# Performance work log

Hardware: AMD Instinct MI355X
Metric: run time of the kernel (lower is better)

Reference implementation:

```python
import jax, jax.numpy as jnp
import numpy as np

# Mamba hyperparameters (match init_kwargs)
DIM = 384
D_STATE = 16
D_CONV = 4
EXPAND = 2
D_INNER = EXPAND * DIM            # 768
DT_RANK = (DIM + 15) // 16        # ceil(dim/16) = 24


def setup_inputs() -> dict:
    key = jax.random.key(0)
    ks = jax.random.split(key, 9)
    B = 4
    img_dims = (16, 16, 16)
    s = 0.02
    x = jax.random.normal(ks[0], (B, DIM) + img_dims, dtype=jnp.float32)
    # LayerNorm params
    gamma = jnp.ones((DIM,), jnp.float32)
    beta = jnp.zeros((DIM,), jnp.float32)
    # Mamba params (torch Linear layout: (out, in))
    W_in = jax.random.normal(ks[1], (2 * D_INNER, DIM), jnp.float32) * s
    conv_w = jax.random.normal(ks[2], (D_INNER, 1, D_CONV), jnp.float32) * (D_CONV ** -0.5)
    conv_b = jnp.zeros((D_INNER,), jnp.float32)
    W_xproj = jax.random.normal(ks[3], (DT_RANK + 2 * D_STATE, D_INNER), jnp.float32) * s
    W_dt = jax.random.normal(ks[4], (D_INNER, DT_RANK), jnp.float32) * (DT_RANK ** -0.5)
    # bias init so softplus(b_dt) gives small positive dt (~0.02), like mamba_ssm
    b_dt = jnp.full((D_INNER,), -4.0, jnp.float32) + jax.random.normal(ks[5], (D_INNER,), jnp.float32) * 0.1
    # S4D-real init: A = -[1..d_state] per channel
    A_log = jnp.log(jnp.broadcast_to(jnp.arange(1, D_STATE + 1, dtype=jnp.float32), (D_INNER, D_STATE)))
    D = jnp.ones((D_INNER,), jnp.float32)
    W_out = jax.random.normal(ks[6], (DIM, D_INNER), jnp.float32) * s
    return {"x": x, "gamma": gamma, "beta": beta, "W_in": W_in, "conv_w": conv_w,
            "conv_b": conv_b, "W_xproj": W_xproj, "W_dt": W_dt, "b_dt": b_dt,
            "A_log": A_log, "D": D, "W_out": W_out}


def _mamba_layer(x, gamma, beta, W_in, conv_w, conv_b, W_xproj, W_dt, b_dt, A_log, D, W_out):
    B, C = x.shape[0], x.shape[1]
    img_dims = x.shape[2:]
    L = int(np.prod(img_dims))
    xf = x.reshape(B, C, L).transpose(0, 2, 1)          # (B, L, C)

    # LayerNorm over channel dim
    mu = xf.mean(-1, keepdims=True)
    xc = xf - mu
    var = (xc * xc).mean(-1, keepdims=True)
    xn = xc * jax.lax.rsqrt(var + 1e-5) * gamma + beta   # (B, L, C)

    # in_proj -> x, z branches
    xz = xn @ W_in.T                                     # (B, L, 2*D_INNER)
    xm, z = jnp.split(xz, 2, axis=-1)

    # causal depthwise conv1d + SiLU
    xcv = xm.transpose(0, 2, 1)                          # (B, D_INNER, L)
    conv = jax.lax.conv_general_dilated(
        xcv, conv_w, window_strides=(1,), padding=[(D_CONV - 1, 0)],
        feature_group_count=D_INNER) + conv_b[None, :, None]
    xm = jax.nn.silu(conv.transpose(0, 2, 1))            # (B, L, D_INNER)

    # input-dependent dt, B, C
    dbl = xm @ W_xproj.T                                 # (B, L, DT_RANK + 2*D_STATE)
    dt, Bm, Cm = jnp.split(dbl, [DT_RANK, DT_RANK + D_STATE], axis=-1)
    delta = jax.nn.softplus(dt @ W_dt.T + b_dt)          # (B, L, D_INNER)
    A = -jnp.exp(A_log)                                  # (D_INNER, D_STATE)

    # selective scan over time (time-major)
    def step(h, inp):
        d_t, x_t, B_t, C_t = inp                         # (B,Din),(B,Din),(B,Dst),(B,Dst)
        dA = jnp.exp(d_t[..., None] * A)                 # (B, D_INNER, D_STATE)
        h = h * dA + (d_t * x_t)[..., None] * B_t[:, None, :]
        y = jnp.einsum('bds,bs->bd', h, C_t)
        return h, y

    h0 = jnp.zeros((B, D_INNER, D_STATE), xm.dtype)
    inps = (delta.transpose(1, 0, 2), xm.transpose(1, 0, 2),
            Bm.transpose(1, 0, 2), Cm.transpose(1, 0, 2))
    _, ys = jax.lax.scan(step, h0, inps)                 # (L, B, D_INNER)

    y = ys.transpose(1, 0, 2) + xm * D                   # skip via D
    y = y * jax.nn.silu(z)                               # gate
    out = y @ W_out.T                                    # (B, L, C)
    return out.transpose(0, 2, 1).reshape(x.shape)


def reference(x, gamma, beta, W_in, conv_w, conv_b, W_xproj, W_dt, b_dt, A_log, D, W_out):
    return _mamba_layer(x, gamma, beta, W_in, conv_w, conv_b, W_xproj, W_dt, b_dt, A_log, D, W_out)
```

## Files before the change

### kernel.cpp

```cpp
#include <hip/hip_runtime.h>

typedef short v8s __attribute__((ext_vector_type(8)));
typedef float v4f __attribute__((ext_vector_type(4)));

#define LSEQ   4096
#define BATCH  4
#define NDIM   384
#define DIN    768
#define DST    16
#define DTR    24
#define NTOK   (BATCH * LSEQ)
#define NCHUNK 128
#define CLEN   32
#define CT     8

__device__ __forceinline__ float b2f(unsigned short u) {
  unsigned int v = ((unsigned int)u) << 16;
  float f; __builtin_memcpy(&f, &v, 4); return f;
}
__device__ __forceinline__ unsigned short f2b(float f) {
  unsigned int x; __builtin_memcpy(&x, &f, 4);
  unsigned int r = x + 0x7FFFu + ((x >> 16) & 1u);
  return (unsigned short)(r >> 16);
}
__device__ __forceinline__ void gl2lds16(const void* g, void* l) {
  __builtin_amdgcn_global_load_lds(
      (const __attribute__((address_space(1))) void*)g,
      (__attribute__((address_space(3))) void*)l, 16, 0, 0);
}

__global__ __launch_bounds__(256) void cast_w(
    const float* __restrict__ a, unsigned short* __restrict__ oa, int na,
    const float* __restrict__ b, unsigned short* __restrict__ ob, int nb,
    const float* __restrict__ c, unsigned short* __restrict__ oc, int nc,
    const float* __restrict__ wdt, unsigned short* __restrict__ odt)
{
  int i = blockIdx.x * 256 + threadIdx.x;
  if (i < na) oa[i] = f2b(a[i]);
  if (i < nb) ob[i] = f2b(b[i]);
  if (i < nc) oc[i] = f2b(c[i]);
  if (i < DIN * 32) {
    int n = i >> 5, r = i & 31;
    odt[i] = (r < DTR) ? f2b(wdt[n * DTR + r]) : (unsigned short)0;
  }
}

__global__ __launch_bounds__(256) void ln_stats(
    const float* __restrict__ x, float* __restrict__ mu, float* __restrict__ rs)
{
  __shared__ float red[512];
  int blk = blockIdx.x;
  int b = blk >> 7, lc = blk & 127;
  int l0 = lc * 32;
  int t = threadIdx.x;
  int lt = t & 31, part = t >> 5;
  float s = 0.f, ss = 0.f;
  for (int c = part; c < NDIM; c += 8) {
    float v = x[((size_t)b * NDIM + c) * LSEQ + l0 + lt];
    s += v; ss += v * v;
  }
  red[part * 32 + lt] = s;
  red[256 + part * 32 + lt] = ss;
  __syncthreads();
  if (t < 32) {
    float sum = 0.f, ssum = 0.f;
    #pragma unroll
    for (int k = 0; k < 8; k++) { sum += red[k * 32 + t]; ssum += red[256 + k * 32 + t]; }
    float m = sum / (float)NDIM;
    float var = ssum / (float)NDIM - m * m;
    mu[(size_t)b * LSEQ + l0 + t] = m;
    rs[(size_t)b * LSEQ + l0 + t] = rsqrtf(var + 1e-5f);
  }
}

__global__ __launch_bounds__(256) void ln_apply(
    const float* __restrict__ x, const float* __restrict__ mu,
    const float* __restrict__ rs, const float* __restrict__ gamma,
    const float* __restrict__ beta, unsigned short* __restrict__ xn)
{
  __shared__ unsigned short tile[64 * 66];
  int blk = blockIdx.x;
  int ltb = blk & 63, ct = (blk >> 6) % 6, b = blk / (6 * 64);
  int l0 = ltb * 64, c0 = ct * 64;
  int t = threadIdx.x;
  int col = (t & 15) * 4;
  float4 mu4 = *(const float4*)(mu + (size_t)b * LSEQ + l0 + col);
  float4 rs4 = *(const float4*)(rs + (size_t)b * LSEQ + l0 + col);
  #pragma unroll
  for (int p = 0; p < 4; p++) {
    int row = (t >> 4) + p * 16;
    float g = gamma[c0 + row], be = beta[c0 + row];
    float4 v = *(const float4*)(x + ((size_t)b * NDIM + c0 + row) * LSEQ + l0 + col);
    unsigned int u0 = (unsigned int)f2b((v.x - mu4.x) * rs4.x * g + be)
                    | ((unsigned int)f2b((v.y - mu4.y) * rs4.y * g + be) << 16);
    unsigned int u1 = (unsigned int)f2b((v.z - mu4.z) * rs4.z * g + be)
                    | ((unsigned int)f2b((v.w - mu4.w) * rs4.w * g + be) << 16);
    *(unsigned int*)&tile[row * 66 + col]     = u0;
    *(unsigned int*)&tile[row * 66 + col + 2] = u1;
  }
  __syncthreads();
  for (int idx = t; idx < 64 * 64; idx += 256) {
    int l = idx >> 6, c = idx & 63;
    xn[((size_t)b * LSEQ + l0 + l) * NDIM + c0 + c] = tile[c * 66 + l];
  }
}

template <typename OT>
__global__ __launch_bounds__(256) void gemm128(
    const unsigned short* __restrict__ A, const unsigned short* __restrict__ W,
    OT* __restrict__ C, int K, int ldc)
{
  __shared__ short As[128 * 32];
  __shared__ short Ws[128 * 32];
  int t = threadIdx.x;
  int wave = t >> 6, lane = t & 63;
  int m0 = blockIdx.x * 128, n0 = blockIdx.y * 128;
  int wm = wave >> 1, wn = wave & 1;
  int lrow = lane & 15, quad = lane >> 4;
  int l4 = lane >> 2, p = lane & 3;
  int row0 = wave * 32 + l4;
  int row1 = row0 + 16;
  int k8 = p ^ (row0 & 3);
  int ldsoff0 = wave * 1024 + lane * 8;
  int ldsoff1 = ldsoff0 + 512;
  int swz = (lrow & 3) * 8;
  v4f acc[4][4];
  #pragma unroll
  for (int i = 0; i < 4; i++)
    #pragma unroll
    for (int j = 0; j < 4; j++) acc[i][j] = (v4f){0.f, 0.f, 0.f, 0.f};
  for (int kk = 0; kk < K; kk += 32) {
    gl2lds16(A + (size_t)(m0 + row0) * K + kk + k8 * 8, &As[ldsoff0]);
    gl2lds16(A + (size_t)(m0 + row1) * K + kk + k8 * 8, &As[ldsoff1]);
    gl2lds16(W + (size_t)(n0 + row0) * K + kk + k8 * 8, &Ws[ldsoff0]);
    gl2lds16(W + (size_t)(n0 + row1) * K + kk + k8 * 8, &Ws[ldsoff1]);
    __syncthreads();
    v8s af[4], bf[4];
    #pragma unroll
    for (int i = 0; i < 4; i++) {
      int ra = wm * 64 + i * 16 + lrow;
      af[i] = *(const v8s*)&As[ra * 32 + ((quad * 8) ^ swz)];
    }
    #pragma unroll
    for (int j = 0; j < 4; j++) {
      int rb = wn * 64 + j * 16 + lrow;
      bf[j] = *(const v8s*)&Ws[rb * 32 + ((quad * 8) ^ swz)];
    }
    #pragma unroll
    for (int i = 0; i < 4; i++)
      #pragma unroll
      for (int j = 0; j < 4; j++)
        acc[i][j] = __builtin_amdgcn_mfma_f32_16x16x32_bf16(af[i], bf[j], acc[i][j], 0, 0, 0);
    __syncthreads();
  }
  #pragma unroll
  for (int i = 0; i < 4; i++) {
    #pragma unroll
    for (int j = 0; j < 4; j++) {
      #pragma unroll
      for (int r = 0; r < 4; r++) {
        int m = m0 + wm * 64 + i * 16 + quad * 4 + r;
        int n = n0 + wn * 64 + j * 16 + lrow;
        if constexpr (sizeof(OT) == 4) C[(size_t)m * ldc + n] = acc[i][j][r];
        else                           C[(size_t)m * ldc + n] = (OT)f2b(acc[i][j][r]);
      }
    }
  }
}

__global__ __launch_bounds__(256) void gemm_out(
    const unsigned short* __restrict__ A, const unsigned short* __restrict__ W,
    float* __restrict__ out, int K)
{
  __shared__ short As[128 * 32];
  __shared__ short Ws[128 * 32];
  int t = threadIdx.x;
  int wave = t >> 6, lane = t & 63;
  int m0 = blockIdx.x * 128, n0 = blockIdx.y * 128;
  int wm = wave >> 1, wn = wave & 1;
  int lrow = lane & 15, quad = lane >> 4;
  int l4 = lane >> 2, p = lane & 3;
  int row0 = wave * 32 + l4;
  int row1 = row0 + 16;
  int k8 = p ^ (row0 & 3);
  int ldsoff0 = wave * 1024 + lane * 8;
  int ldsoff1 = ldsoff0 + 512;
  int swz = (lrow & 3) * 8;
  v4f acc[4][4];
  #pragma unroll
  for (int i = 0; i < 4; i++)
    #pragma unroll
    for (int j = 0; j < 4; j++) acc[i][j] = (v4f){0.f, 0.f, 0.f, 0.f};
  for (int kk = 0; kk < K; kk += 32) {
    gl2lds16(A + (size_t)(m0 + row0) * K + kk + k8 * 8, &As[ldsoff0]);
    gl2lds16(A + (size_t)(m0 + row1) * K + kk + k8 * 8, &As[ldsoff1]);
    gl2lds16(W + (size_t)(n0 + row0) * K + kk + k8 * 8, &Ws[ldsoff0]);
    gl2lds16(W + (size_t)(n0 + row1) * K + kk + k8 * 8, &Ws[ldsoff1]);
    __syncthreads();
    v8s af[4], bf[4];
    #pragma unroll
    for (int i = 0; i < 4; i++) {
      int ra = wm * 64 + i * 16 + lrow;
      af[i] = *(const v8s*)&As[ra * 32 + ((quad * 8) ^ swz)];
    }
    #pragma unroll
    for (int j = 0; j < 4; j++) {
      int rb = wn * 64 + j * 16 + lrow;
      bf[j] = *(const v8s*)&Ws[rb * 32 + ((quad * 8) ^ swz)];
    }
    #pragma unroll
    for (int i = 0; i < 4; i++)
      #pragma unroll
      for (int j = 0; j < 4; j++)
        acc[i][j] = __builtin_amdgcn_mfma_f32_16x16x32_bf16(af[i], bf[j], acc[i][j], 0, 0, 0);
    __syncthreads();
  }
  #pragma unroll
  for (int i = 0; i < 4; i++) {
    #pragma unroll
    for (int j = 0; j < 4; j++) {
      #pragma unroll
      for (int r = 0; r < 4; r++) {
        int m = m0 + wm * 64 + i * 16 + quad * 4 + r;
        int n = n0 + wn * 64 + j * 16 + lrow;
        int b = n >> 12, l = n & (LSEQ - 1);
        out[((size_t)b * NDIM + m) * LSEQ + l] = acc[i][j][r];
      }
    }
  }
}

#define LDK 40
__global__ __launch_bounds__(256) void gemm_bt64(
    const unsigned short* __restrict__ A, const unsigned short* __restrict__ W,
    unsigned short* __restrict__ C, int Nw, int K, int ldc)
{
  __shared__ short As[64 * LDK];
  __shared__ short Ws[64 * LDK];
  int m0 = blockIdx.x * 64, n0 = blockIdx.y * 64;
  int t = threadIdx.x;
  int wave = t >> 6, lane = t & 63;
  int lrow = lane & 15, quad = lane >> 4;
  int ldrow = t >> 2, ldcg = t & 3;
  v4f acc[4];
  #pragma unroll
  for (int j = 0; j < 4; j++) acc[j] = (v4f){0.f, 0.f, 0.f, 0.f};
  for (int kk = 0; kk < K; kk += 32) {
    v8s av = *(const v8s*)(A + (size_t)(m0 + ldrow) * K + kk + ldcg * 8);
    *(v8s*)&As[ldrow * LDK + ldcg * 8] = av;
    int wrow = n0 + ldrow;
    v8s wv = {0, 0, 0, 0, 0, 0, 0, 0};
    if (wrow < Nw) wv = *(const v8s*)(W + (size_t)wrow * K + kk + ldcg * 8);
    *(v8s*)&Ws[ldrow * LDK + ldcg * 8] = wv;
    __syncthreads();
    v8s afrag = *(const v8s*)&As[(wave * 16 + lrow) * LDK + quad * 8];
    #pragma unroll
    for (int j = 0; j < 4; j++) {
      v8s bfrag = *(const v8s*)&Ws[(j * 16 + lrow) * LDK + quad * 8];
      acc[j] = __builtin_amdgcn_mfma_f32_16x16x32_bf16(afrag, bfrag, acc[j], 0, 0, 0);
    }
    __syncthreads();
  }
  #pragma unroll
  for (int j = 0; j < 4; j++) {
    #pragma unroll
    for (int r = 0; r < 4; r++) {
      int m = m0 + wave * 16 + quad * 4 + r;
      int n = n0 + j * 16 + lrow;
      if (n < ldc) C[(size_t)m * ldc + n] = f2b(acc[j][r]);
    }
  }
}

__global__ __launch_bounds__(256) void dt_gemm(
    const unsigned short* __restrict__ A, const unsigned short* __restrict__ W,
    const float* __restrict__ b_dt, unsigned short* __restrict__ delta)
{
  __shared__ short As[128 * 32];
  __shared__ short Ws[128 * 32];
  int t = threadIdx.x;
  int wave = t >> 6, lane = t & 63;
  int m0 = blockIdx.x * 128, n0 = blockIdx.y * 128;
  int wm = wave >> 1, wn = wave & 1;
  int lrow = lane & 15, quad = lane >> 4;
  int l4 = lane >> 2, p = lane & 3;
  int row0 = wave * 32 + l4;
  int row1 = row0 + 16;
  int k8 = p ^ (row0 & 3);
  int ldsoff0 = wave * 1024 + lane * 8;
  int ldsoff1 = ldsoff0 + 512;
  int swz = (lrow & 3) * 8;
  gl2lds16(A + (size_t)(m0 + row0) * 64 + k8 * 8, &As[ldsoff0]);
  gl2lds16(A + (size_t)(m0 + row1) * 64 + k8 * 8, &As[ldsoff1]);
  gl2lds16(W + (size_t)(n0 + row0) * 32 + k8 * 8, &Ws[ldsoff0]);
  gl2lds16(W + (size_t)(n0 + row1) * 32 + k8 * 8, &Ws[ldsoff1]);
  __syncthreads();
  v4f acc[4][4];
  #pragma unroll
  for (int i = 0; i < 4; i++)
    #pragma unroll
    for (int j = 0; j < 4; j++) acc[i][j] = (v4f){0.f, 0.f, 0.f, 0.f};
  v8s af[4], bf[4];
  #pragma unroll
  for (int i = 0; i < 4; i++) {
    int ra = wm * 64 + i * 16 + lrow;
    af[i] = *(const v8s*)&As[ra * 32 + ((quad * 8) ^ swz)];
  }
  #pragma unroll
  for (int j = 0; j < 4; j++) {
    int rb = wn * 64 + j * 16 + lrow;
    bf[j] = *(const v8s*)&Ws[rb * 32 + ((quad * 8) ^ swz)];
  }
  #pragma unroll
  for (int i = 0; i < 4; i++)
    #pragma unroll
    for (int j = 0; j < 4; j++)
      acc[i][j] = __builtin_amdgcn_mfma_f32_16x16x32_bf16(af[i], bf[j], acc[i][j], 0, 0, 0);
  #pragma unroll
  for (int j = 0; j < 4; j++) {
    int n = n0 + wn * 64 + j * 16 + lrow;
    float bb = b_dt[n];
    #pragma unroll
    for (int i = 0; i < 4; i++) {
      #pragma unroll
      for (int r = 0; r < 4; r++) {
        int m = m0 + wm * 64 + i * 16 + quad * 4 + r;
        float a = acc[i][j][r] + bb;
        float sp = (a > 20.f) ? a : __logf(1.f + __expf(a));
        delta[(size_t)m * DIN + n] = f2b(sp);
      }
    }
  }
}

__global__ __launch_bounds__(256) void conv_silu_w(
    const unsigned short* __restrict__ xz, const float* __restrict__ conv_w,
    const float* __restrict__ conv_b, unsigned short* __restrict__ xc)
{
  int idx = blockIdx.x * 256 + threadIdx.x;
  int dg = idx % (DIN / 8);
  int bl0 = idx / (DIN / 8);
  int d = dg * 8;
  int t0 = bl0 * CT;
  int l0 = t0 & (LSEQ - 1);
  float w[4][8], bb[8];
  #pragma unroll
  for (int e = 0; e < 8; e++) {
    float4 we = *(const float4*)(conv_w + (size_t)(d + e) * 4);
    w[0][e] = we.x; w[1][e] = we.y; w[2][e] = we.z; w[3][e] = we.w;
  }
  {
    float4 b0 = *(const float4*)(conv_b + d);
    float4 b1 = *(const float4*)(conv_b + d + 4);
    bb[0] = b0.x; bb[1] = b0.y; bb[2] = b0.z; bb[3] = b0.w;
    bb[4] = b1.x; bb[5] = b1.y; bb[6] = b1.z; bb[7] = b1.w;
  }
  float xw[3][8];
  #pragma unroll
  for (int j = 0; j < 3; j++) {
    if (l0 - 3 + j >= 0) {
      v8s v = *(const v8s*)(xz + (size_t)(t0 - 3 + j) * (2 * DIN) + d);
      #pragma unroll
      for (int e = 0; e < 8; e++) xw[j][e] = b2f((unsigned short)v[e]);
    } else {
      #pragma unroll
      for (int e = 0; e < 8; e++) xw[j][e] = 0.f;
    }
  }
  for (int tt = 0; tt < CT; tt++) {
    v8s v = *(const v8s*)(xz + (size_t)(t0 + tt) * (2 * DIN) + d);
    float cur[8];
    #pragma unroll
    for (int e = 0; e < 8; e++) cur[e] = b2f((unsigned short)v[e]);
    v8s o;
    #pragma unroll
    for (int e = 0; e < 8; e++) {
      float acc = bb[e];
      acc = __builtin_fmaf(w[0][e], xw[0][e], acc);
      acc = __builtin_fmaf(w[1][e], xw[1][e], acc);
      acc = __builtin_fmaf(w[2][e], xw[2][e], acc);
      acc = __builtin_fmaf(w[3][e], cur[e], acc);
      float sig = 1.f / (1.f + __expf(-acc));
      o[e] = (short)f2b(acc * sig);
    }
    *(v8s*)(xc + (size_t)(t0 + tt) * DIN + d) = o;
    #pragma unroll
    for (int e = 0; e < 8; e++) {
      xw[0][e] = xw[1][e]; xw[1][e] = xw[2][e]; xw[2][e] = cur[e];
    }
  }
}

__global__ __launch_bounds__(256) void scan_a(
    const unsigned short* __restrict__ delta, const unsigned short* __restrict__ xc,
    const unsigned short* __restrict__ dbl, const float* __restrict__ A_log,
    float* __restrict__ P, float* __restrict__ H)
{
  __shared__ float BCf[CLEN * 32];
  int blk = blockIdx.x;
  int q = blk % 3, c = (blk / 3) % NCHUNK, b = blk / (3 * NCHUNK);
  int t = threadIdx.x;
  int d = q * 256 + t;
  if (t < CLEN * 4) {
    int tt = t >> 2, g = t & 3;
    v8s raw = *(const v8s*)(dbl + (size_t)(b * LSEQ + c * CLEN + tt) * 64 + DTR + g * 8);
    float* dst = &BCf[tt * 32 + g * 8];
    #pragma unroll
    for (int e = 0; e < 8; e++) dst[e] = b2f((unsigned short)raw[e]);
  }
  __syncthreads();
  float A_d[DST];
  bool fast = true;
  #pragma unroll
  for (int s = 0; s < DST; s++) {
    A_d[s] = -__expf(A_log[d * DST + s]);
    fast = fast && (__builtin_fabsf(A_d[s] + (float)(s + 1)) < 1e-3f * (s + 1));
  }
  float h[DST];
  #pragma unroll
  for (int s = 0; s < DST; s++) h[s] = 0.f;
  float S = 0.f;
  size_t base = ((size_t)b * LSEQ + c * CLEN) * DIN + d;
  if (fast) {
    for (int tt = 0; tt < CLEN; tt++) {
      float du = b2f(delta[base + (size_t)tt * DIN]);
      float xv = b2f(xc[base + (size_t)tt * DIN]);
      float dx = du * xv;
      S += du;
      float r = __expf(-du);
      float Bv[16];
      #pragma unroll
      for (int g = 0; g < 4; g++)
        *(float4*)&Bv[g * 4] = *(const float4*)&BCf[tt * 32 + g * 4];
      float a = r;
      #pragma unroll
      for (int s = 0; s < DST; s++) {
        h[s] = __builtin_fmaf(h[s], a, dx * Bv[s]);
        a *= r;
      }
    }
  } else {
    for (int tt = 0; tt < CLEN; tt++) {
      float du = b2f(delta[base + (size_t)tt * DIN]);
      float xv = b2f(xc[base + (size_t)tt * DIN]);
      float dx = du * xv;
      S += du;
      #pragma unroll
      for (int s = 0; s < DST; s++) {
        float a = __expf(du * A_d[s]);
        h[s] = h[s] * a + dx * BCf[tt * 32 + s];
      }
    }
  }
  size_t obase = (((size_t)b * NCHUNK + c) * DST) * DIN + d;
  if (fast) {
    float rS = __expf(-S), a = rS;
    #pragma unroll
    for (int s = 0; s < DST; s++) { P[obase + (size_t)s * DIN] = a; a *= rS; }
  } else {
    #pragma unroll
    for (int s = 0; s < DST; s++) P[obase + (size_t)s * DIN] = __expf(A_d[s] * S);
  }
  #pragma unroll
  for (int s = 0; s < DST; s++) H[obase + (size_t)s * DIN] = h[s];
}

__global__ __launch_bounds__(256) void scan_b(
    const float* __restrict__ P, const float* __restrict__ H, float* __restrict__ Hstart)
{
  int i = blockIdx.x * 256 + threadIdx.x;
  if (i >= BATCH * DST * DIN) return;
  int d = i % DIN;
  int s = (i / DIN) % DST;
  int b = i / (DST * DIN);
  float h = 0.f;
  for (int c = 0; c < NCHUNK; c++) {
    size_t idx = (((size_t)b * NCHUNK + c) * DST + s) * DIN + d;
    float p = P[idx];
    float hh = H[idx];
    Hstart[idx] = h;
    h = h * p + hh;
  }
}

__global__ __launch_bounds__(256) void scan_c(
    const unsigned short* __restrict__ delta, const unsigned short* __restrict__ xc,
    const unsigned short* __restrict__ dbl, const float* __restrict__ A_log,
    const float* __restrict__ Hstart, const unsigned short* __restrict__ xz,
    const float* __restrict__ Dp, unsigned short* __restrict__ ygate)
{
  __shared__ float BCf[CLEN * 32];
  int blk = blockIdx.x;
  int q = blk % 3, c = (blk / 3) % NCHUNK, b = blk / (3 * NCHUNK);
  int t = threadIdx.x;
  int d = q * 256 + t;
  if (t < CLEN * 4) {
    int tt = t >> 2, g = t & 3;
    v8s raw = *(const v8s*)(dbl + (size_t)(b * LSEQ + c * CLEN + tt) * 64 + DTR + g * 8);
    float* dst = &BCf[tt * 32 + g * 8];
    #pragma unroll
    for (int e = 0; e < 8; e++) dst[e] = b2f((unsigned short)raw[e]);
  }
  __syncthreads();
  float A_d[DST];
  bool fast = true;
  #pragma unroll
  for (int s = 0; s < DST; s++) {
    A_d[s] = -__expf(A_log[d * DST + s]);
    fast = fast && (__builtin_fabsf(A_d[s] + (float)(s + 1)) < 1e-3f * (s + 1));
  }
  size_t obase = (((size_t)b * NCHUNK + c) * DST) * DIN + d;
  float h[DST];
  #pragma unroll
  for (int s = 0; s < DST; s++) h[s] = Hstart[obase + (size_t)s * DIN];
  float Dv = Dp[d];
  size_t base = ((size_t)b * LSEQ + c * CLEN) * DIN + d;
  size_t zbase = ((size_t)b * LSEQ + c * CLEN) * (2 * DIN) + DIN + d;
  if (fast) {
    for (int tt = 0; tt < CLEN; tt++) {
      float du = b2f(delta[base + (size_t)tt * DIN]);
      float xv = b2f(xc[base + (size_t)tt * DIN]);
      float dx = du * xv;
      float r = __expf(-du);
      float Bv[16], Cv[16];
      #pragma unroll
      for (int g = 0; g < 4; g++) {
        *(float4*)&Bv[g * 4] = *(const float4*)&BCf[tt * 32 + g * 4];
        *(float4*)&Cv[g * 4] = *(const float4*)&BCf[tt * 32 + 16 + g * 4];
      }
      float a = r, y = 0.f;
      #pragma unroll
      for (int s = 0; s < DST; s++) {
        h[s] = __builtin_fmaf(h[s], a, dx * Bv[s]);
        y = __builtin_fmaf(h[s], Cv[s], y);
        a *= r;
      }
      float zv = b2f(xz[zbase + (size_t)tt * (2 * DIN)]);
      float g = zv / (1.f + __expf(-zv));
      float o = (y + xv * Dv) * g;
      ygate[base + (size_t)tt * DIN] = f2b(o);
    }
  } else {
    for (int tt = 0; tt < CLEN; tt++) {
      float du = b2f(delta[base + (size_t)tt * DIN]);
      float xv = b2f(xc[base + (size_t)tt * DIN]);
      float dx = du * xv;
      float y = 0.f;
      #pragma unroll
      for (int s = 0; s < DST; s++) {
        float a = __expf(du * A_d[s]);
        h[s] = h[s] * a + dx * BCf[tt * 32 + s];
        y += h[s] * BCf[tt * 32 + 16 + s];
      }
      float zv = b2f(xz[zbase + (size_t)tt * (2 * DIN)]);
      float g = zv / (1.f + __expf(-zv));
      float o = (y + xv * Dv) * g;
      ygate[base + (size_t)tt * DIN] = f2b(o);
    }
  }
}

extern "C" void kernel_launch(void* const* d_in, const int* in_sizes, int n_in,
                              void* d_out, int out_size, void* d_ws, size_t ws_size,
                              hipStream_t stream) {
  const float* x      = (const float*)d_in[0];
  const float* gamma  = (const float*)d_in[1];
  const float* beta   = (const float*)d_in[2];
  const float* W_in   = (const float*)d_in[3];
  const float* conv_w = (const float*)d_in[4];
  const float* conv_b = (const float*)d_in[5];
  const float* W_xprj = (const float*)d_in[6];
  const float* W_dt   = (const float*)d_in[7];
  const float* b_dt   = (const float*)d_in[8];
  const float* A_log  = (const float*)d_in[9];
  const float* Dp     = (const float*)d_in[10];
  const float* W_out  = (const float*)d_in[11];
  float* out = (float*)d_out;

  char* ws = (char*)d_ws;
  size_t off = 0;
  auto take = [&](size_t bytes) -> char* {
    char* p = ws + off;
    off = (off + bytes + 255) & ~(size_t)255;
    return p;
  };
  const int NW_IN = 2 * DIN * NDIM;
  const int NW_XP = 56 * DIN;
  const int NW_OUT = NDIM * DIN;
  unsigned short* Wc_in  = (unsigned short*)take((size_t)NW_IN * 2);
  unsigned short* Wc_xp  = (unsigned short*)take((size_t)NW_XP * 2);
  unsigned short* Wc_out = (unsigned short*)take((size_t)NW_OUT * 2);
  unsigned short* Wc_dt  = (unsigned short*)take((size_t)DIN * 32 * 2);
  float*          mu    = (float*)take((size_t)NTOK * 4);
  float*          rsb   = (float*)take((size_t)NTOK * 4);
  unsigned short* xn    = (unsigned short*)take((size_t)NTOK * NDIM * 2);
  unsigned short* xz    = (unsigned short*)take((size_t)NTOK * 2 * DIN * 2);
  unsigned short* xc    = (unsigned short*)take((size_t)NTOK * DIN * 2);
  unsigned short* dbl   = (unsigned short*)take((size_t)NTOK * 64 * 2);
  unsigned short* delta = (unsigned short*)take((size_t)NTOK * DIN * 2);
  unsigned short* ygate = (unsigned short*)take((size_t)NTOK * DIN * 2);
  float*          P     = (float*)take((size_t)BATCH * NCHUNK * DST * DIN * 4);
  float*          H     = (float*)take((size_t)BATCH * NCHUNK * DST * DIN * 4);
  float*          Hst   = P;
  (void)ws_size; (void)in_sizes; (void)n_in; (void)out_size;

  cast_w<<<(NW_IN + 255) / 256, 256, 0, stream>>>(W_in, Wc_in, NW_IN,
                                                  W_xprj, Wc_xp, NW_XP,
                                                  W_out, Wc_out, NW_OUT,
                                                  W_dt, Wc_dt);
  ln_stats<<<BATCH * (LSEQ / 32), 256, 0, stream>>>(x, mu, rsb);
  ln_apply<<<BATCH * 6 * (LSEQ / 64), 256, 0, stream>>>(x, mu, rsb, gamma, beta, xn);
  gemm128<unsigned short><<<dim3(NTOK / 128, 1536 / 128), 256, 0, stream>>>(xn, Wc_in, xz, NDIM, 1536);
  conv_silu_w<<<(NTOK / CT) * (DIN / 8) / 256, 256, 0, stream>>>(xz, conv_w, conv_b, xc);
  gemm_bt64<<<dim3(NTOK / 64, 1), 256, 0, stream>>>(xc, Wc_xp, dbl, 56, DIN, 64);
  dt_gemm<<<dim3(NTOK / 128, DIN / 128), 256, 0, stream>>>(dbl, Wc_dt, b_dt, delta);
  scan_a<<<BATCH * NCHUNK * 3, 256, 0, stream>>>(delta, xc, dbl, A_log, P, H);
  scan_b<<<(BATCH * DST * DIN + 255) / 256, 256, 0, stream>>>(P, H, Hst);
  scan_c<<<BATCH * NCHUNK * 3, 256, 0, stream>>>(delta, xc, dbl, A_log, Hst, xz, Dp, ygate);
  gemm_out<<<dim3(NDIM / 128, NTOK / 128), 256, 0, stream>>>(Wc_out, ygate, out, DIN);
}
```

Measured before the change: 308.6 us.

## Fuse weight cast with LN stats, store chunk delta sums, split decay chains

After: 313.7 us. Within noise of the previous version (+1.6%).

```diff
diff --git a/kernel.cpp b/kernel.cpp
--- a/kernel.cpp
+++ b/kernel.cpp
@@ -29,34 +29,35 @@
       (__attribute__((address_space(3))) void*)l, 16, 0, 0);
 }
 
-__global__ __launch_bounds__(256) void cast_w(
+#define CAST_BLOCKS 2304
+
+__global__ __launch_bounds__(256) void cast_ln(
     const float* __restrict__ a, unsigned short* __restrict__ oa, int na,
     const float* __restrict__ b, unsigned short* __restrict__ ob, int nb,
     const float* __restrict__ c, unsigned short* __restrict__ oc, int nc,
-    const float* __restrict__ wdt, unsigned short* __restrict__ odt)
-{
-  int i = blockIdx.x * 256 + threadIdx.x;
-  if (i < na) oa[i] = f2b(a[i]);
-  if (i < nb) ob[i] = f2b(b[i]);
-  if (i < nc) oc[i] = f2b(c[i]);
-  if (i < DIN * 32) {
-    int n = i >> 5, r = i & 31;
-    odt[i] = (r < DTR) ? f2b(wdt[n * DTR + r]) : (unsigned short)0;
-  }
-}
-
-__global__ __launch_bounds__(256) void ln_stats(
+    const float* __restrict__ wdt, unsigned short* __restrict__ odt,
     const float* __restrict__ x, float* __restrict__ mu, float* __restrict__ rs)
 {
   __shared__ float red[512];
-  int blk = blockIdx.x;
-  int b = blk >> 7, lc = blk & 127;
+  int t = threadIdx.x;
+  if (blockIdx.x < CAST_BLOCKS) {
+    int i = blockIdx.x * 256 + t;
+    if (i < na) oa[i] = f2b(a[i]);
+    if (i < nb) ob[i] = f2b(b[i]);
+    if (i < nc) oc[i] = f2b(c[i]);
+    if (i < DIN * 32) {
+      int n = i >> 5, r = i & 31;
+      odt[i] = (r < DTR) ? f2b(wdt[n * DTR + r]) : (unsigned short)0;
+    }
+    return;
+  }
+  int blk = blockIdx.x - CAST_BLOCKS;
+  int bb = blk >> 7, lc = blk & 127;
   int l0 = lc * 32;
-  int t = threadIdx.x;
   int lt = t & 31, part = t >> 5;
   float s = 0.f, ss = 0.f;
-  for (int c = part; c < NDIM; c += 8) {
-    float v = x[((size_t)b * NDIM + c) * LSEQ + l0 + lt];
+  for (int ch = part; ch < NDIM; ch += 8) {
+    float v = x[((size_t)bb * NDIM + ch) * LSEQ + l0 + lt];
     s += v; ss += v * v;
   }
   red[part * 32 + lt] = s;
@@ -68,8 +69,8 @@
     for (int k = 0; k < 8; k++) { sum += red[k * 32 + t]; ssum += red[256 + k * 32 + t]; }
     float m = sum / (float)NDIM;
     float var = ssum / (float)NDIM - m * m;
-    mu[(size_t)b * LSEQ + l0 + t] = m;
-    rs[(size_t)b * LSEQ + l0 + t] = rsqrtf(var + 1e-5f);
+    mu[(size_t)bb * LSEQ + l0 + t] = m;
+    rs[(size_t)bb * LSEQ + l0 + t] = rsqrtf(var + 1e-5f);
   }
 }
 
@@ -394,7 +395,7 @@
 __global__ __launch_bounds__(256) void scan_a(
     const unsigned short* __restrict__ delta, const unsigned short* __restrict__ xc,
     const unsigned short* __restrict__ dbl, const float* __restrict__ A_log,
-    float* __restrict__ P, float* __restrict__ H)
+    float* __restrict__ Ssum, float* __restrict__ H)
 {
   __shared__ float BCf[CLEN * 32];
   int blk = blockIdx.x;
@@ -416,30 +417,41 @@
     A_d[s] = -__expf(A_log[d * DST + s]);
     fast = fast && (__builtin_fabsf(A_d[s] + (float)(s + 1)) < 1e-3f * (s + 1));
   }
-  float h[DST];
-  #pragma unroll
-  for (int s = 0; s < DST; s++) h[s] = 0.f;
   float S = 0.f;
   size_t base = ((size_t)b * LSEQ + c * CLEN) * DIN + d;
+  size_t obase = (((size_t)b * NCHUNK + c) * DST) * DIN + d;
   if (fast) {
+    float hx[8], hy[8];
+    #pragma unroll
+    for (int i = 0; i < 8; i++) { hx[i] = 0.f; hy[i] = 0.f; }
     for (int tt = 0; tt < CLEN; tt++) {
       float du = b2f(delta[base + (size_t)tt * DIN]);
       float xv = b2f(xc[base + (size_t)tt * DIN]);
       float dx = du * xv;
       S += du;
       float r = __expf(-du);
+      float r2 = r * r;
       float Bv[16];
       #pragma unroll
       for (int g = 0; g < 4; g++)
         *(float4*)&Bv[g * 4] = *(const float4*)&BCf[tt * 32 + g * 4];
-      float a = r;
-      #pragma unroll
-      for (int s = 0; s < DST; s++) {
-        h[s] = __builtin_fmaf(h[s], a, dx * Bv[s]);
-        a *= r;
-      }
+      float ax = r, ay = r2;
+      #pragma unroll
+      for (int i = 0; i < 8; i++) {
+        hx[i] = __builtin_fmaf(hx[i], ax, dx * Bv[2 * i]);
+        hy[i] = __builtin_fmaf(hy[i], ay, dx * Bv[2 * i + 1]);
+        ax *= r2; ay *= r2;
+      }
+    }
+    #pragma unroll
+    for (int i = 0; i < 8; i++) {
+      H[obase + (size_t)(2 * i) * DIN] = hx[i];
+      H[obase + (size_t)(2 * i + 1) * DIN] = hy[i];
     }
   } else {
+    float h[DST];
+    #pragma unroll
+    for (int s = 0; s < DST; s++) h[s] = 0.f;
     for (int tt = 0; tt < CLEN; tt++) {
       float du = b2f(delta[base + (size_t)tt * DIN]);
       float xv = b2f(xc[base + (size_t)tt * DIN]);
@@ -451,35 +463,29 @@
         h[s] = h[s] * a + dx * BCf[tt * 32 + s];
       }
     }
-  }
-  size_t obase = (((size_t)b * NCHUNK + c) * DST) * DIN + d;
-  if (fast) {
-    float rS = __expf(-S), a = rS;
-    #pragma unroll
-    for (int s = 0; s < DST; s++) { P[obase + (size_t)s * DIN] = a; a *= rS; }
-  } else {
-    #pragma unroll
-    for (int s = 0; s < DST; s++) P[obase + (size_t)s * DIN] = __expf(A_d[s] * S);
-  }
-  #pragma unroll
-  for (int s = 0; s < DST; s++) H[obase + (size_t)s * DIN] = h[s];
+    #pragma unroll
+    for (int s = 0; s < DST; s++) H[obase + (size_t)s * DIN] = h[s];
+  }
+  Ssum[((size_t)b * NCHUNK + c) * DIN + d] = S;
 }
 
 __global__ __launch_bounds__(256) void scan_b(
-    const float* __restrict__ P, const float* __restrict__ H, float* __restrict__ Hstart)
+    const float* __restrict__ Ssum, const float* __restrict__ H,
+    const float* __restrict__ A_log, float* __restrict__ Hstart)
 {
   int i = blockIdx.x * 256 + threadIdx.x;
   if (i >= BATCH * DST * DIN) return;
   int d = i % DIN;
   int s = (i / DIN) % DST;
   int b = i / (DST * DIN);
+  float A_d = -__expf(A_log[d * DST + s]);
   float h = 0.f;
   for (int c = 0; c < NCHUNK; c++) {
     size_t idx = (((size_t)b * NCHUNK + c) * DST + s) * DIN + d;
-    float p = P[idx];
+    float S = Ssum[((size_t)b * NCHUNK + c) * DIN + d];
     float hh = H[idx];
     Hstart[idx] = h;
-    h = h * p + hh;
+    h = h * __expf(A_d * S) + hh;
   }
 }
 
@@ -510,37 +516,47 @@
     fast = fast && (__builtin_fabsf(A_d[s] + (float)(s + 1)) < 1e-3f * (s + 1));
   }
   size_t obase = (((size_t)b * NCHUNK + c) * DST) * DIN + d;
-  float h[DST];
-  #pragma unroll
-  for (int s = 0; s < DST; s++) h[s] = Hstart[obase + (size_t)s * DIN];
   float Dv = Dp[d];
   size_t base = ((size_t)b * LSEQ + c * CLEN) * DIN + d;
   size_t zbase = ((size_t)b * LSEQ + c * CLEN) * (2 * DIN) + DIN + d;
   if (fast) {
+    float hx[8], hy[8];
+    #pragma unroll
+    for (int i = 0; i < 8; i++) {
+      hx[i] = Hstart[obase + (size_t)(2 * i) * DIN];
+      hy[i] = Hstart[obase + (size_t)(2 * i + 1) * DIN];
+    }
     for (int tt = 0; tt < CLEN; tt++) {
       float du = b2f(delta[base + (size_t)tt * DIN]);
       float xv = b2f(xc[base + (size_t)tt * DIN]);
       float dx = du * xv;
       float r = __expf(-du);
+      float r2 = r * r;
       float Bv[16], Cv[16];
       #pragma unroll
       for (int g = 0; g < 4; g++) {
         *(float4*)&Bv[g * 4] = *(const float4*)&BCf[tt * 32 + g * 4];
         *(float4*)&Cv[g * 4] = *(const float4*)&BCf[tt * 32 + 16 + g * 4];
       }
-      float a = r, y = 0.f;
-      #pragma unroll
-      for (int s = 0; s < DST; s++) {
-        h[s] = __builtin_fmaf(h[s], a, dx * Bv[s]);
-        y = __builtin_fmaf(h[s], Cv[s], y);
-        a *= r;
-      }
+      float ax = r, ay = r2, yx = 0.f, yy = 0.f;
+      #pragma unroll
+      for (int i = 0; i < 8; i++) {
+        hx[i] = __builtin_fmaf(hx[i], ax, dx * Bv[2 * i]);
+        hy[i] = __builtin_fmaf(hy[i], ay, dx * Bv[2 * i + 1]);
+        yx = __builtin_fmaf(hx[i], Cv[2 * i], yx);
+        yy = __builtin_fmaf(hy[i], Cv[2 * i + 1], yy);
+        ax *= r2; ay *= r2;
+      }
+      float y = yx + yy;
       float zv = b2f(xz[zbase + (size_t)tt * (2 * DIN)]);
       float g = zv / (1.f + __expf(-zv));
       float o = (y + xv * Dv) * g;
       ygate[base + (size_t)tt * DIN] = f2b(o);
     }
   } else {
+    float h[DST];
+    #pragma unroll
+    for (int s = 0; s < DST; s++) h[s] = Hstart[obase + (size_t)s * DIN];
     for (int tt = 0; tt < CLEN; tt++) {
       float du = b2f(delta[base + (size_t)tt * DIN]);
       float xv = b2f(xc[base + (size_t)tt * DIN]);
@@ -599,23 +615,21 @@
   unsigned short* dbl   = (unsigned short*)take((size_t)NTOK * 64 * 2);
   unsigned short* delta = (unsigned short*)take((size_t)NTOK * DIN * 2);
   unsigned short* ygate = (unsigned short*)take((size_t)NTOK * DIN * 2);
-  float*          P     = (float*)take((size_t)BATCH * NCHUNK * DST * DIN * 4);
+  float*          Ssum  = (float*)take((size_t)BATCH * NCHUNK * DIN * 4);
   float*          H     = (float*)take((size_t)BATCH * NCHUNK * DST * DIN * 4);
-  float*          Hst   = P;
+  float*          Hst   = (float*)take((size_t)BATCH * NCHUNK * DST * DIN * 4);
   (void)ws_size; (void)in_sizes; (void)n_in; (void)out_size;
 
-  cast_w<<<(NW_IN + 255) / 256, 256, 0, stream>>>(W_in, Wc_in, NW_IN,
-                                                  W_xprj, Wc_xp, NW_XP,
-                                                  W_out, Wc_out, NW_OUT,
-                                                  W_dt, Wc_dt);
-  ln_stats<<<BATCH * (LSEQ / 32), 256, 0, stream>>>(x, mu, rsb);
+  cast_ln<<<CAST_BLOCKS + BATCH * (LSEQ / 32), 256, 0, stream>>>(
+      W_in, Wc_in, NW_IN, W_xprj, Wc_xp, NW_XP, W_out, Wc_out, NW_OUT,
+      W_dt, Wc_dt, x, mu, rsb);
   ln_apply<<<BATCH * 6 * (LSEQ / 64), 256, 0, stream>>>(x, mu, rsb, gamma, beta, xn);
   gemm128<unsigned short><<<dim3(NTOK / 128, 1536 / 128), 256, 0, stream>>>(xn, Wc_in, xz, NDIM, 1536);
   conv_silu_w<<<(NTOK / CT) * (DIN / 8) / 256, 256, 0, stream>>>(xz, conv_w, conv_b, xc);
   gemm_bt64<<<dim3(NTOK / 64, 1), 256, 0, stream>>>(xc, Wc_xp, dbl, 56, DIN, 64);
   dt_gemm<<<dim3(NTOK / 128, DIN / 128), 256, 0, stream>>>(dbl, Wc_dt, b_dt, delta);
-  scan_a<<<BATCH * NCHUNK * 3, 256, 0, stream>>>(delta, xc, dbl, A_log, P, H);
-  scan_b<<<(BATCH * DST * DIN + 255) / 256, 256, 0, stream>>>(P, H, Hst);
+  scan_a<<<BATCH * NCHUNK * 3, 256, 0, stream>>>(delta, xc, dbl, A_log, Ssum, H);
+  scan_b<<<(BATCH * DST * DIN + 255) / 256, 256, 0, stream>>>(Ssum, H, A_log, Hst);
   scan_c<<<BATCH * NCHUNK * 3, 256, 0, stream>>>(delta, xc, dbl, A_log, Hst, xz, Dp, ygate);
   gemm_out<<<dim3(NDIM / 128, NTOK / 128), 256, 0, stream>>>(Wc_out, ygate, out, DIN);
 }
```
